# Kernel optimization log

Hardware: AMD Instinct MI355X
Metric: run time of the kernel (lower is better)

## Reference

```python
import jax, jax.numpy as jnp
import numpy as np

B, L, C = 4, 16384, 512   # batch, tokens (128x128 grid), dim
NH, WS = 8, 8             # num_heads, window grid (ws)
HD = C // NH              # head_dim = 64


def setup_inputs() -> dict:
    key = jax.random.key(0)
    k1, k2, k3, k4, k5 = jax.random.split(key, 5)
    return {
        "q":   jax.random.normal(k1, (B, L, C), dtype=jnp.float32),
        "kv":  jax.random.normal(k2, (B, L, C), dtype=jnp.float32),
        "Wq":  jax.random.normal(k3, (C, C), dtype=jnp.float32) * 0.02,
        "Wkv": jax.random.normal(k4, (C, 2 * C), dtype=jnp.float32) * 0.02,
        "Wfc": jax.random.normal(k5, (C, C), dtype=jnp.float32) * 0.02,
    }


def reference(q, kv, Wq, Wkv, Wfc):
    Bq, Lq, Cd = q.shape
    Lkv = kv.shape[1]
    nh, hd, ws = NH, Cd // NH, WS
    scale = hd ** (-0.5)
    hw_q = int(round(Lq ** 0.5))   # 128
    hw_k = int(round(Lkv ** 0.5))
    sq, sk = hw_q // ws, hw_k // ws  # window side lengths (16)

    qp = q @ Wq                                   # [B, Lq, C]
    kvp = (kv @ Wkv).reshape(Bq, Lkv, 2, Cd)
    k, v = kvp[:, :, 0], kvp[:, :, 1]             # [B, Lkv, C]

    def window(x, s):
        # [B, hw, hw, C] -> [B, ws*ws windows, heads, s*s tokens, hd]
        x = x.reshape(Bq, ws, s, ws, s, Cd).transpose(0, 1, 3, 2, 4, 5)
        x = x.reshape(Bq, ws * ws, s * s, nh, hd)
        return x.transpose(0, 1, 3, 2, 4)

    qw = window(qp, sq)   # [B, W, H, sq*sq, hd]
    kw = window(k, sk)    # [B, W, H, sk*sk, hd]
    vw = window(v, sk)

    attn = jnp.einsum('bwhqd,bwhkd->bwhqk', qw, kw) * scale
    attn = jax.nn.softmax(attn, axis=-1)
    o = jnp.einsum('bwhqk,bwhkd->bwhqd', attn, vw)  # [B, W, H, sq*sq, hd]

    # inverse window partition
    o = o.transpose(0, 1, 3, 2, 4).reshape(Bq, ws, ws, sq, sq, Cd)
    o = o.transpose(0, 1, 3, 2, 4, 5).reshape(Bq, Lq, Cd)
    return o @ Wfc
```

## Files before the change

### kernel.cpp

```cpp
#include <hip/hip_runtime.h>
#include <stdint.h>

#define BB 4
#define LL 16384
#define CC 512
#define MM (BB * LL)

typedef unsigned short u16;
typedef __bf16 bf16x8 __attribute__((ext_vector_type(8)));
typedef float f32x4 __attribute__((ext_vector_type(4)));
typedef u16 u16x8 __attribute__((ext_vector_type(8)));
typedef u16 u16x4 __attribute__((ext_vector_type(4)));

__device__ __forceinline__ u16 f2bf(float f) {
  return __builtin_bit_cast(u16, (__bf16)f);
}

__device__ __forceinline__ void gl_lds16(const void* g, void* l) {
  __builtin_amdgcn_global_load_lds((const __attribute__((address_space(1))) void*)g,
                                   (__attribute__((address_space(3))) void*)l,
                                   16, 0, 0);
}

__global__ __launch_bounds__(256) void prep_kernel(
    const float* __restrict__ q, const float* __restrict__ kv,
    const float* __restrict__ Wq, const float* __restrict__ Wkv,
    const float* __restrict__ Wfc, u16* __restrict__ qo, u16* __restrict__ kvo,
    u16* __restrict__ Wq_t, u16* __restrict__ Wkv_t, u16* __restrict__ Wfc_t) {
  __shared__ float tile[64][65];
  const int bid = blockIdx.x, tid = threadIdx.x;

  if (bid < 4096) {
    const int half = bid >> 11;
    const float* src = half ? kv : q;
    u16* dst = half ? kvo : qo;
    const int n16 = MM * CC / 16;
    const int stride = 2048 * 256;
    for (int i = (bid & 2047) * 256 + tid; i < n16; i += stride) {
      const f32x4* sp = reinterpret_cast<const f32x4*>(src) + 4 * i;
      f32x4 a0 = __builtin_nontemporal_load(sp + 0);
      f32x4 a1 = __builtin_nontemporal_load(sp + 1);
      f32x4 a2 = __builtin_nontemporal_load(sp + 2);
      f32x4 a3 = __builtin_nontemporal_load(sp + 3);
      u16x8 o0, o1;
      o0[0] = f2bf(a0[0]); o0[1] = f2bf(a0[1]); o0[2] = f2bf(a0[2]); o0[3] = f2bf(a0[3]);
      o0[4] = f2bf(a1[0]); o0[5] = f2bf(a1[1]); o0[6] = f2bf(a1[2]); o0[7] = f2bf(a1[3]);
      o1[0] = f2bf(a2[0]); o1[1] = f2bf(a2[1]); o1[2] = f2bf(a2[2]); o1[3] = f2bf(a2[3]);
      o1[4] = f2bf(a3[0]); o1[5] = f2bf(a3[1]); o1[6] = f2bf(a3[2]); o1[7] = f2bf(a3[3]);
      reinterpret_cast<u16x8*>(dst)[2 * i + 0] = o0;
      reinterpret_cast<u16x8*>(dst)[2 * i + 1] = o1;
    }
    return;
  }

  const int wb = bid - 4096;
  const float* W; u16* Wt; int N, ti;
  if (wb < 64)       { W = Wq;  Wt = Wq_t;  N = 512;  ti = wb; }
  else if (wb < 192) { W = Wkv; Wt = Wkv_t; N = 1024; ti = wb - 64; }
  else               { W = Wfc; Wt = Wfc_t; N = 512;  ti = wb - 192; }
  const int ntn = N >> 6;
  const int kt = ti / ntn, nt = ti % ntn;
  const int k0 = kt << 6, n0 = nt << 6;
  {
    const int r = tid >> 4, c4 = tid & 15;
#pragma unroll
    for (int e = 0; e < 4; ++e) {
      int row = r + e * 16;
      f32x4 v = *reinterpret_cast<const f32x4*>(&W[(size_t)(k0 + row) * N + n0 + c4 * 4]);
      tile[row][c4 * 4 + 0] = v[0]; tile[row][c4 * 4 + 1] = v[1];
      tile[row][c4 * 4 + 2] = v[2]; tile[row][c4 * 4 + 3] = v[3];
    }
  }
  __syncthreads();
  {
    const int n = tid >> 2, qd = tid & 3;
#pragma unroll
    for (int e = 0; e < 2; ++e) {
      int c = qd * 2 + e;
      u16x8 o;
#pragma unroll
      for (int j = 0; j < 8; ++j) o[j] = f2bf(tile[c * 8 + j][n]);
      *reinterpret_cast<u16x8*>(&Wt[(size_t)(n0 + n) * 512 + k0 + c * 8]) = o;
    }
  }
}

template <bool OUT_F32>
__global__ __launch_bounds__(256, 3) void gemm128(const u16* __restrict__ A,
                                                  const u16* __restrict__ Bt,
                                                  void* __restrict__ Cp,
                                                  int N, int nbnl) {
  constexpr int K = 512;
  constexpr int NT = 8;
  __shared__ __align__(16) u16 Al[2][8192];
  __shared__ __align__(16) u16 Bl[8192];
  const int nwg = gridDim.x;
  const int bid0 = blockIdx.x;
  const int cpx = nwg >> 3;
  const int bid = (bid0 & 7) * cpx + (bid0 >> 3);
  const int bm = bid >> nbnl, bn = bid & ((1 << nbnl) - 1);
  const size_t row0 = (size_t)bm << 7, col0 = (size_t)bn << 7;
  const int tid = threadIdx.x, lane = tid & 63;
  const int wv = tid >> 6, wm = wv >> 1, wn = wv & 1;
  const int ro = lane & 15, g4 = lane >> 4;

  auto stageA = [&](int kt, u16* L) {
#pragma unroll
    for (int c = 0; c < 4; ++c) {
      int cc = tid + c * 256;
      int r = cc >> 3, g = (cc & 7) ^ (r & 7);
      gl_lds16(A + (row0 + r) * (size_t)K + kt * 64 + g * 8, L + cc * 8);
    }
  };
  auto stageB = [&](int kt) {
#pragma unroll
    for (int c = 0; c < 4; ++c) {
      int cc = tid + c * 256;
      int r = cc >> 3, g = (cc & 7) ^ (r & 7);
      gl_lds16(Bt + (col0 + r) * (size_t)K + kt * 64 + g * 8, Bl + cc * 8);
    }
  };

  const int aB = (wm * 64 + ro) * 64;
  const int bB = (wn * 64 + ro) * 64;
  const int sw0 = (g4 ^ (ro & 7)) * 8;
  const int sw1 = ((g4 + 4) ^ (ro & 7)) * 8;

  auto ldf = [&](const u16* p) { return *reinterpret_cast<const bf16x8*>(p); };

  f32x4 acc[4][4] = {};

  stageA(0, Al[0]); stageB(0);
  asm volatile("s_waitcnt vmcnt(0)" ::: "memory");
  __builtin_amdgcn_s_barrier();

  for (int u = 0; u < NT; ++u) {
    u16* LA = Al[u & 1];
    u16* LAn = Al[(u + 1) & 1];
    const bool st = (u + 1) < NT;
    bf16x8 bfr[4][2], af[2][2];

#pragma unroll
    for (int n = 0; n < 4; ++n) {
      bfr[n][0] = ldf(Bl + bB + n * 1024 + sw0);
      bfr[n][1] = ldf(Bl + bB + n * 1024 + sw1);
    }
    af[0][0] = ldf(LA + aB + sw0);        af[0][1] = ldf(LA + aB + sw1);
    af[1][0] = ldf(LA + aB + 1024 + sw0); af[1][1] = ldf(LA + aB + 1024 + sw1);
    if (st) stageA(u + 1, LAn);
    __builtin_amdgcn_s_barrier();
    asm volatile("s_waitcnt lgkmcnt(0)" ::: "memory");
    __builtin_amdgcn_sched_barrier(0);
    __builtin_amdgcn_s_setprio(1);
#pragma unroll
    for (int m = 0; m < 2; ++m)
#pragma unroll
      for (int n = 0; n < 4; ++n) {
        acc[m][n] = __builtin_amdgcn_mfma_f32_16x16x32_bf16(af[m][0], bfr[n][0], acc[m][n], 0, 0, 0);
        acc[m][n] = __builtin_amdgcn_mfma_f32_16x16x32_bf16(af[m][1], bfr[n][1], acc[m][n], 0, 0, 0);
      }
    __builtin_amdgcn_s_setprio(0);
    __builtin_amdgcn_s_barrier();

    af[0][0] = ldf(LA + aB + 2048 + sw0); af[0][1] = ldf(LA + aB + 2048 + sw1);
    af[1][0] = ldf(LA + aB + 3072 + sw0); af[1][1] = ldf(LA + aB + 3072 + sw1);
    if (st) stageB(u + 1);
    __builtin_amdgcn_s_barrier();
    asm volatile("s_waitcnt lgkmcnt(0)" ::: "memory");
    __builtin_amdgcn_sched_barrier(0);
    __builtin_amdgcn_s_setprio(1);
#pragma unroll
    for (int m = 0; m < 2; ++m)
#pragma unroll
      for (int n = 0; n < 4; ++n) {
        acc[2 + m][n] = __builtin_amdgcn_mfma_f32_16x16x32_bf16(af[m][0], bfr[n][0], acc[2 + m][n], 0, 0, 0);
        acc[2 + m][n] = __builtin_amdgcn_mfma_f32_16x16x32_bf16(af[m][1], bfr[n][1], acc[2 + m][n], 0, 0, 0);
      }
    __builtin_amdgcn_s_setprio(0);
    asm volatile("s_waitcnt vmcnt(0)" ::: "memory");
    __builtin_amdgcn_s_barrier();
  }

#pragma unroll
  for (int m = 0; m < 4; ++m)
#pragma unroll
    for (int n = 0; n < 4; ++n)
#pragma unroll
      for (int j = 0; j < 4; ++j) {
        size_t r = row0 + wm * 64 + m * 16 + g4 * 4 + j;
        size_t c = col0 + wn * 64 + n * 16 + ro;
        if (OUT_F32)
          reinterpret_cast<float*>(Cp)[r * N + c] = acc[m][n][j];
        else
          reinterpret_cast<u16*>(Cp)[r * N + c] = f2bf(acc[m][n][j]);
      }
}

__global__ __launch_bounds__(512, 4) void attn_kernel(const u16* __restrict__ qp,
                                                      const u16* __restrict__ kvp,
                                                      u16* __restrict__ o) {
  __shared__ __align__(16) u16 Kl[256 * 64];
  __shared__ __align__(16) u16 Vt[64 * 256];
  __shared__ __align__(16) u16 Pl[8 * 1024];
  const int bid = blockIdx.x;
  const int h = bid & 7, w = (bid >> 3) & 63, b = bid >> 9;
  const int w1 = w >> 3, w2 = w & 7;
  const int tid = threadIdx.x, lane = tid & 63, wv = tid >> 6;

  auto lrow = [&](int t) { return (w1 * 16 + (t >> 4)) * 128 + w2 * 16 + (t & 15); };

#pragma unroll
  for (int p = 0; p < 4; ++p) {
    int ci = tid + p * 512;
    int r = ci >> 3, g = (ci & 7) ^ (r & 7);
    gl_lds16(kvp + ((size_t)(b * LL + lrow(r))) * 1024 + h * 64 + g * 8, Kl + ci * 8);
  }
  {
    const int tk = tid >> 1, half = tid & 1;
    const size_t base = ((size_t)(b * LL + lrow(tk))) * 1024 + 512 + h * 64 + half * 32;
#pragma unroll
    for (int c = 0; c < 4; ++c) {
      u16x8 vx = *reinterpret_cast<const u16x8*>(kvp + base + c * 8);
#pragma unroll
      for (int e = 0; e < 8; ++e) {
        int d = half * 32 + c * 8 + e;
        Vt[d * 256 + (((tk >> 3) ^ (d & 7)) * 8) + (tk & 7)] = vx[e];
      }
    }
  }
  __syncthreads();

  const int ro = lane & 15;
  const int g4 = lane >> 4;
  const float scale = 0.125f;
  const int swA = (g4 ^ (ro & 7)) * 8;
  const int swB = ((g4 + 4) ^ (ro & 7)) * 8;
  u16* PW = Pl + wv * 1024;

  auto ldf = [&](const u16* p) { return *reinterpret_cast<const bf16x8*>(p); };

#pragma unroll
  for (int rt = 0; rt < 2; ++rt) {
    const int tq = 32 * wv + 16 * rt + ro;
    const size_t qbase = ((size_t)(b * LL + lrow(tq))) * 512 + h * 64 + g4 * 8;
    const bf16x8 qf0 = *reinterpret_cast<const bf16x8*>(qp + qbase);
    const bf16x8 qf1 = *reinterpret_cast<const bf16x8*>(qp + qbase + 32);

    f32x4 sa[16] = {};
    __builtin_amdgcn_s_setprio(1);
#pragma unroll
    for (int ct = 0; ct < 16; ++ct) {
      bf16x8 kf0 = ldf(Kl + (16 * ct + ro) * 64 + swA);
      bf16x8 kf1 = ldf(Kl + (16 * ct + ro) * 64 + swB);
      sa[ct] = __builtin_amdgcn_mfma_f32_16x16x32_bf16(qf0, kf0, sa[ct], 0, 0, 0);
      sa[ct] = __builtin_amdgcn_mfma_f32_16x16x32_bf16(qf1, kf1, sa[ct], 0, 0, 0);
    }
    __builtin_amdgcn_s_setprio(0);

#pragma unroll
    for (int j = 0; j < 4; ++j) {
      float m = -1e30f;
#pragma unroll
      for (int ct = 0; ct < 16; ++ct) m = fmaxf(m, sa[ct][j]);
      m = fmaxf(m, __shfl_xor(m, 1));
      m = fmaxf(m, __shfl_xor(m, 2));
      m = fmaxf(m, __shfl_xor(m, 4));
      m = fmaxf(m, __shfl_xor(m, 8));
      m *= scale;
      float s = 0.f;
#pragma unroll
      for (int ct = 0; ct < 16; ++ct) {
        float p = __expf(sa[ct][j] * scale - m);
        sa[ct][j] = p;
        s += p;
      }
      s += __shfl_xor(s, 1);
      s += __shfl_xor(s, 2);
      s += __shfl_xor(s, 4);
      s += __shfl_xor(s, 8);
      float inv = 1.f / s;
#pragma unroll
      for (int ct = 0; ct < 16; ++ct) sa[ct][j] *= inv;
    }

    f32x4 oacc[4] = {};
#pragma unroll
    for (int kh = 0; kh < 4; ++kh) {
#pragma unroll
      for (int c = 0; c < 4; ++c)
#pragma unroll
        for (int j = 0; j < 4; ++j) {
          int rq = g4 * 4 + j;
          PW[rq * 64 + (((2 * c + (ro >> 3)) ^ (rq & 7)) * 8) + (ro & 7)] =
              f2bf(sa[kh * 4 + c][j]);
        }
      __builtin_amdgcn_s_setprio(1);
#pragma unroll
      for (int ks = 0; ks < 2; ++ks) {
        bf16x8 pf = ldf(PW + ro * 64 + (((ks * 4 + g4) ^ (ro & 7)) * 8));
        const int kkg = kh * 2 + ks;
#pragma unroll
        for (int cd = 0; cd < 4; ++cd) {
          bf16x8 vf = ldf(Vt + (16 * cd + ro) * 256 + (((kkg * 4 + g4) ^ (ro & 7)) * 8));
          oacc[cd] = __builtin_amdgcn_mfma_f32_16x16x32_bf16(pf, vf, oacc[cd], 0, 0, 0);
        }
      }
      __builtin_amdgcn_s_setprio(0);
    }

#pragma unroll
    for (int cd = 0; cd < 4; ++cd)
#pragma unroll
      for (int j = 0; j < 4; ++j) {
        int t = 32 * wv + 16 * rt + g4 * 4 + j;
        int d = 16 * cd + ro;
        o[((size_t)(b * LL + lrow(t))) * 512 + h * 64 + d] = f2bf(oacc[cd][j]);
      }
  }
}

extern "C" void kernel_launch(void* const* d_in, const int* in_sizes, int n_in,
                              void* d_out, int out_size, void* d_ws, size_t ws_size,
                              hipStream_t stream) {
  const float* q = (const float*)d_in[0];
  const float* kv = (const float*)d_in[1];
  const float* Wq = (const float*)d_in[2];
  const float* Wkv = (const float*)d_in[3];
  const float* Wfc = (const float*)d_in[4];
  float* out = (float*)d_out;
  char* ws = (char*)d_ws;

  u16* q_bf  = (u16*)(ws + 0);
  u16* kv_bf = (u16*)(ws + 67108864);
  u16* qp    = (u16*)(ws + 134217728);
  u16* kvp   = (u16*)(ws + 201326592);
  u16* Wq_t  = (u16*)(ws + 335544320);
  u16* Wkv_t = (u16*)(ws + 336068608);
  u16* Wfc_t = (u16*)(ws + 337117184);
  u16* o_buf = q_bf;

  prep_kernel<<<4352, 256, 0, stream>>>(q, kv, Wq, Wkv, Wfc, q_bf, kv_bf, Wq_t, Wkv_t, Wfc_t);

  gemm128<false><<<2048, 256, 0, stream>>>(q_bf, Wq_t, qp, CC, 2);
  gemm128<false><<<4096, 256, 0, stream>>>(kv_bf, Wkv_t, kvp, 2 * CC, 3);

  attn_kernel<<<BB * 64 * 8, 512, 0, stream>>>(qp, kvp, o_buf);

  gemm128<true><<<2048, 256, 0, stream>>>(o_buf, Wfc_t, out, CC, 2);
}
```

Before: 366.7 us.

## Fuse fp32-to-bf16 activation conversion into projection GEMM A-tile loads

```diff
diff --git a/kernel.cpp b/kernel.cpp
--- a/kernel.cpp
+++ b/kernel.cpp
@@ -22,42 +22,18 @@
                                    16, 0, 0);
 }
 
-__global__ __launch_bounds__(256) void prep_kernel(
-    const float* __restrict__ q, const float* __restrict__ kv,
-    const float* __restrict__ Wq, const float* __restrict__ Wkv,
-    const float* __restrict__ Wfc, u16* __restrict__ qo, u16* __restrict__ kvo,
-    u16* __restrict__ Wq_t, u16* __restrict__ Wkv_t, u16* __restrict__ Wfc_t) {
+__global__ __launch_bounds__(256) void tcvt_kernel(const float* __restrict__ Wq,
+                                                   const float* __restrict__ Wkv,
+                                                   const float* __restrict__ Wfc,
+                                                   u16* __restrict__ Wq_t,
+                                                   u16* __restrict__ Wkv_t,
+                                                   u16* __restrict__ Wfc_t) {
   __shared__ float tile[64][65];
   const int bid = blockIdx.x, tid = threadIdx.x;
-
-  if (bid < 4096) {
-    const int half = bid >> 11;
-    const float* src = half ? kv : q;
-    u16* dst = half ? kvo : qo;
-    const int n16 = MM * CC / 16;
-    const int stride = 2048 * 256;
-    for (int i = (bid & 2047) * 256 + tid; i < n16; i += stride) {
-      const f32x4* sp = reinterpret_cast<const f32x4*>(src) + 4 * i;
-      f32x4 a0 = __builtin_nontemporal_load(sp + 0);
-      f32x4 a1 = __builtin_nontemporal_load(sp + 1);
-      f32x4 a2 = __builtin_nontemporal_load(sp + 2);
-      f32x4 a3 = __builtin_nontemporal_load(sp + 3);
-      u16x8 o0, o1;
-      o0[0] = f2bf(a0[0]); o0[1] = f2bf(a0[1]); o0[2] = f2bf(a0[2]); o0[3] = f2bf(a0[3]);
-      o0[4] = f2bf(a1[0]); o0[5] = f2bf(a1[1]); o0[6] = f2bf(a1[2]); o0[7] = f2bf(a1[3]);
-      o1[0] = f2bf(a2[0]); o1[1] = f2bf(a2[1]); o1[2] = f2bf(a2[2]); o1[3] = f2bf(a2[3]);
-      o1[4] = f2bf(a3[0]); o1[5] = f2bf(a3[1]); o1[6] = f2bf(a3[2]); o1[7] = f2bf(a3[3]);
-      reinterpret_cast<u16x8*>(dst)[2 * i + 0] = o0;
-      reinterpret_cast<u16x8*>(dst)[2 * i + 1] = o1;
-    }
-    return;
-  }
-
-  const int wb = bid - 4096;
   const float* W; u16* Wt; int N, ti;
-  if (wb < 64)       { W = Wq;  Wt = Wq_t;  N = 512;  ti = wb; }
-  else if (wb < 192) { W = Wkv; Wt = Wkv_t; N = 1024; ti = wb - 64; }
-  else               { W = Wfc; Wt = Wfc_t; N = 512;  ti = wb - 192; }
+  if (bid < 64)       { W = Wq;  Wt = Wq_t;  N = 512;  ti = bid; }
+  else if (bid < 192) { W = Wkv; Wt = Wkv_t; N = 1024; ti = bid - 64; }
+  else                { W = Wfc; Wt = Wfc_t; N = 512;  ti = bid - 192; }
   const int ntn = N >> 6;
   const int kt = ti / ntn, nt = ti % ntn;
   const int k0 = kt << 6, n0 = nt << 6;
@@ -85,8 +61,8 @@
   }
 }
 
-template <bool OUT_F32>
-__global__ __launch_bounds__(256, 3) void gemm128(const u16* __restrict__ A,
+template <bool A_F32, bool OUT_F32>
+__global__ __launch_bounds__(256, 3) void gemm128(const void* __restrict__ Ap,
                                                   const u16* __restrict__ Bt,
                                                   void* __restrict__ Cp,
                                                   int N, int nbnl) {
@@ -94,6 +70,8 @@
   constexpr int NT = 8;
   __shared__ __align__(16) u16 Al[2][8192];
   __shared__ __align__(16) u16 Bl[8192];
+  const u16* A16 = (const u16*)Ap;
+  const float* A32 = (const float*)Ap;
   const int nwg = gridDim.x;
   const int bid0 = blockIdx.x;
   const int cpx = nwg >> 3;
@@ -104,12 +82,12 @@
   const int wv = tid >> 6, wm = wv >> 1, wn = wv & 1;
   const int ro = lane & 15, g4 = lane >> 4;
 
-  auto stageA = [&](int kt, u16* L) {
+  auto stageA16 = [&](int kt, u16* L) {
 #pragma unroll
     for (int c = 0; c < 4; ++c) {
       int cc = tid + c * 256;
       int r = cc >> 3, g = (cc & 7) ^ (r & 7);
-      gl_lds16(A + (row0 + r) * (size_t)K + kt * 64 + g * 8, L + cc * 8);
+      gl_lds16(A16 + (row0 + r) * (size_t)K + kt * 64 + g * 8, L + cc * 8);
     }
   };
   auto stageB = [&](int kt) {
@@ -118,6 +96,28 @@
       int cc = tid + c * 256;
       int r = cc >> 3, g = (cc & 7) ^ (r & 7);
       gl_lds16(Bt + (col0 + r) * (size_t)K + kt * 64 + g * 8, Bl + cc * 8);
+    }
+  };
+
+  f32x4 av[4][2];
+  auto aloadR = [&](int kt) {
+#pragma unroll
+    for (int c = 0; c < 4; ++c) {
+      int cc = tid + c * 256;
+      int r = cc >> 3, g = (cc & 7) ^ (r & 7);
+      const float* s = A32 + (row0 + r) * (size_t)K + kt * 64 + g * 8;
+      av[c][0] = *reinterpret_cast<const f32x4*>(s);
+      av[c][1] = *reinterpret_cast<const f32x4*>(s + 4);
+    }
+  };
+  auto awrite = [&](u16* L) {
+#pragma unroll
+    for (int c = 0; c < 4; ++c) {
+      int cc = tid + c * 256;
+      bf16x8 w;
+#pragma unroll
+      for (int e = 0; e < 8; ++e) w[e] = (__bf16)av[c][e >> 2][e & 3];
+      *reinterpret_cast<bf16x8*>(L + cc * 8) = w;
     }
   };
 
@@ -130,8 +130,15 @@
 
   f32x4 acc[4][4] = {};
 
-  stageA(0, Al[0]); stageB(0);
-  asm volatile("s_waitcnt vmcnt(0)" ::: "memory");
+  if (A_F32) {
+    aloadR(0); stageB(0);
+    asm volatile("s_waitcnt vmcnt(4)" ::: "memory");
+    awrite(Al[0]);
+    asm volatile("s_waitcnt vmcnt(0) lgkmcnt(0)" ::: "memory");
+  } else {
+    stageA16(0, Al[0]); stageB(0);
+    asm volatile("s_waitcnt vmcnt(0)" ::: "memory");
+  }
   __builtin_amdgcn_s_barrier();
 
   for (int u = 0; u < NT; ++u) {
@@ -147,7 +154,7 @@
     }
     af[0][0] = ldf(LA + aB + sw0);        af[0][1] = ldf(LA + aB + sw1);
     af[1][0] = ldf(LA + aB + 1024 + sw0); af[1][1] = ldf(LA + aB + 1024 + sw1);
-    if (st) stageA(u + 1, LAn);
+    if (st) { if (A_F32) aloadR(u + 1); else stageA16(u + 1, LAn); }
     __builtin_amdgcn_s_barrier();
     asm volatile("s_waitcnt lgkmcnt(0)" ::: "memory");
     __builtin_amdgcn_sched_barrier(0);
@@ -177,6 +184,11 @@
         acc[2 + m][n] = __builtin_amdgcn_mfma_f32_16x16x32_bf16(af[m][1], bfr[n][1], acc[2 + m][n], 0, 0, 0);
       }
     __builtin_amdgcn_s_setprio(0);
+    if (A_F32 && st) {
+      asm volatile("s_waitcnt vmcnt(4)" ::: "memory");
+      awrite(LAn);
+      asm volatile("s_waitcnt lgkmcnt(0)" ::: "memory");
+    }
     asm volatile("s_waitcnt vmcnt(0)" ::: "memory");
     __builtin_amdgcn_s_barrier();
   }
@@ -330,21 +342,19 @@
   float* out = (float*)d_out;
   char* ws = (char*)d_ws;
 
-  u16* q_bf  = (u16*)(ws + 0);
-  u16* kv_bf = (u16*)(ws + 67108864);
+  u16* o_buf = (u16*)(ws + 0);
   u16* qp    = (u16*)(ws + 134217728);
   u16* kvp   = (u16*)(ws + 201326592);
   u16* Wq_t  = (u16*)(ws + 335544320);
   u16* Wkv_t = (u16*)(ws + 336068608);
   u16* Wfc_t = (u16*)(ws + 337117184);
-  u16* o_buf = q_bf;
-
-  prep_kernel<<<4352, 256, 0, stream>>>(q, kv, Wq, Wkv, Wfc, q_bf, kv_bf, Wq_t, Wkv_t, Wfc_t);
-
-  gemm128<false><<<2048, 256, 0, stream>>>(q_bf, Wq_t, qp, CC, 2);
-  gemm128<false><<<4096, 256, 0, stream>>>(kv_bf, Wkv_t, kvp, 2 * CC, 3);
+
+  tcvt_kernel<<<256, 256, 0, stream>>>(Wq, Wkv, Wfc, Wq_t, Wkv_t, Wfc_t);
+
+  gemm128<true, false><<<2048, 256, 0, stream>>>(q, Wq_t, qp, CC, 2);
+  gemm128<true, false><<<4096, 256, 0, stream>>>(kv, Wkv_t, kvp, 2 * CC, 3);
 
   attn_kernel<<<BB * 64 * 8, 512, 0, stream>>>(qp, kvp, o_buf);
 
-  gemm128<true><<<2048, 256, 0, stream>>>(o_buf, Wfc_t, out, CC, 2);
-}
+  gemm128<false, true><<<2048, 256, 0, stream>>>(o_buf, Wfc_t, out, CC, 2);
+}
```

After: 402.5 us. 9.7% more time.
